# Performance work log

Hardware: AMD Instinct MI355X
Metric: run time of the kernel (lower is better)

## Reference

```python
import jax, jax.numpy as jnp
import numpy as np

N, E, B = 4096, 4096, 128  # nodes, edges, graphs


def _param(key, shape, scale):
    return jax.random.normal(key, shape, dtype=jnp.float32) * scale


def setup_inputs() -> dict:
    key = jax.random.key(0)
    ks = jax.random.split(key, 32)
    inp = {
        "x": jax.random.normal(ks[0], (N, 37), dtype=jnp.float32),
        "edge_index": jax.random.randint(ks[1], (2, E), 0, N),
        "edge_attr": jax.random.uniform(ks[2], (E, 5), dtype=jnp.float32),
        "batch": jnp.sort(jax.random.randint(ks[3], (N,), 0, B)),
        # NNConv 1: edge-MLP 5->512->37*128, root [37,128]
        "nn1_w1": _param(ks[4], (5, 512), 0.3),
        "nn1_b1": jnp.zeros((512,), jnp.float32),
        "nn1_w2": _param(ks[5], (512, 37 * 128), 0.01),
        "nn1_b2": jnp.zeros((37 * 128,), jnp.float32),
        "root1": _param(ks[6], (37, 128), 0.1),
        "bias1": jnp.zeros((128,), jnp.float32),
        # NNConv 2: edge-MLP 5->128->128*256, root [128,256]
        "nn2_w1": _param(ks[7], (5, 128), 0.3),
        "nn2_b1": jnp.zeros((128,), jnp.float32),
        "nn2_w2": _param(ks[8], (128, 128 * 256), 0.005),
        "nn2_b2": jnp.zeros((128 * 256,), jnp.float32),
        "root2": _param(ks[9], (128, 256), 0.05),
        "bias2": jnp.zeros((256,), jnp.float32),
        # NNConv 3: edge-MLP 5->128->256*256, root [256,256]
        "nn3_w1": _param(ks[10], (5, 128), 0.3),
        "nn3_b1": jnp.zeros((128,), jnp.float32),
        "nn3_w2": _param(ks[11], (128, 256 * 256), 0.005),
        "nn3_b2": jnp.zeros((256 * 256,), jnp.float32),
        "root3": _param(ks[12], (256, 256), 0.05),
        "bias3": jnp.zeros((256,), jnp.float32),
        # readout MLP
        "fc1_w": _param(ks[13], (256, 128), 0.06),
        "fc1_b": jnp.zeros((128,), jnp.float32),
        "fc2_w": _param(ks[14], (128, 64), 0.09),
        "fc2_b": jnp.zeros((64,), jnp.float32),
        "fc3_w": _param(ks[15], (64, 1), 0.12),
        "fc3_b": jnp.zeros((1,), jnp.float32),
    }
    return inp


def _nnconv(x, src, dst, edge_attr, w1, b1, w2, b2, root, bias, cin, cout):
    # edge MLP -> per-edge weight matrix [E, cin, cout]
    h = jax.nn.relu(edge_attr @ w1 + b1)
    W = (h @ w2 + b2).reshape(-1, cin, cout)
    # gather source features, per-edge matvec, scatter-add to targets
    msg = jnp.einsum('ei,eio->eo', x[src], W)          # [E, cout]
    agg = jax.ops.segment_sum(msg, dst, num_segments=x.shape[0])
    return agg + x @ root + bias


def _segment_mean(x, seg, num_segments):
    s = jax.ops.segment_sum(x, seg, num_segments=num_segments)
    cnt = jax.ops.segment_sum(jnp.ones((x.shape[0],), x.dtype), seg,
                              num_segments=num_segments)
    return s / jnp.maximum(cnt, 1.0)[:, None]


def reference(x, edge_index, edge_attr, batch,
              nn1_w1, nn1_b1, nn1_w2, nn1_b2, root1, bias1,
              nn2_w1, nn2_b1, nn2_w2, nn2_b2, root2, bias2,
              nn3_w1, nn3_b1, nn3_w2, nn3_b2, root3, bias3,
              fc1_w, fc1_b, fc2_w, fc2_b, fc3_w, fc3_b):
    src, dst = edge_index[0], edge_index[1]
    h = jax.nn.elu(_nnconv(x, src, dst, edge_attr, nn1_w1, nn1_b1, nn1_w2,
                           nn1_b2, root1, bias1, 37, 128))
    h = jax.nn.elu(_nnconv(h, src, dst, edge_attr, nn2_w1, nn2_b1, nn2_w2,
                           nn2_b2, root2, bias2, 128, 256))
    h = jax.nn.elu(_nnconv(h, src, dst, edge_attr, nn3_w1, nn3_b1, nn3_w2,
                           nn3_b2, root3, bias3, 256, 256))
    g = _segment_mean(h, batch, B)                     # [B, 256]
    g = jax.nn.elu(g @ fc1_w + fc1_b)
    g = jax.nn.elu(g @ fc2_w + fc2_b)
    g = g @ fc3_w + fc3_b
    return g.reshape(-1)
```

## Files before the change

### kernel.cpp

```cpp
#include <hip/hip_runtime.h>
#include <cstdint>
#include <cstddef>

typedef float f32x4 __attribute__((ext_vector_type(4)));
typedef _Float16 f16x8 __attribute__((ext_vector_type(8)));
typedef _Float16 f16x4 __attribute__((ext_vector_type(4)));
typedef _Float16 f16x2 __attribute__((ext_vector_type(2)));

__device__ __forceinline__ float elu_f(float x) { return x > 0.f ? x : expm1f(x); }

__device__ __forceinline__ void gload_lds16(const void* g, void* l)
{
    __builtin_amdgcn_global_load_lds(
        (const __attribute__((address_space(1))) void*)g,
        (__attribute__((address_space(3))) void*)l,
        16, 0, 0);
}

__global__ __launch_bounds__(256)
void edge_mlp_kernel(const float* __restrict__ ea,
                     const float* __restrict__ w1a, const float* __restrict__ b1a, float* __restrict__ h1T,
                     const float* __restrict__ w1b, const float* __restrict__ b1b, float* __restrict__ h2T,
                     const float* __restrict__ w1c, const float* __restrict__ b1c, float* __restrict__ h3T,
                     int E)
{
    const int e0  = blockIdx.x * 64;
    const int tid = threadIdx.x;
    const int el  = tid & 63;
    const int cg  = tid >> 6;
    __shared__ float a[64][5];
    for (int i = tid; i < 320; i += 256) a[i / 5][i % 5] = ea[e0 * 5 + i];
    __syncthreads();
    float av[5];
    #pragma unroll
    for (int j = 0; j < 5; ++j) av[j] = a[el][j];

    #pragma unroll 4
    for (int t = 0; t < 128; ++t) {
        const int ch = t * 4 + cg;
        float s = b1a[ch];
        #pragma unroll
        for (int j = 0; j < 5; ++j) s = fmaf(av[j], w1a[j * 512 + ch], s);
        h1T[(size_t)ch * E + e0 + el] = fmaxf(s, 0.f);
    }
    #pragma unroll 4
    for (int t = 0; t < 32; ++t) {
        const int ch = t * 4 + cg;
        float s = b1b[ch];
        float u = b1c[ch];
        #pragma unroll
        for (int j = 0; j < 5; ++j) {
            s = fmaf(av[j], w1b[j * 128 + ch], s);
            u = fmaf(av[j], w1c[j * 128 + ch], u);
        }
        h2T[(size_t)ch * E + e0 + el] = fmaxf(s, 0.f);
        h3T[(size_t)ch * E + e0 + el] = fmaxf(u, 0.f);
    }
}

template <int CIN, int COUT, int KFTOT>
__global__ __launch_bounds__(256)
void pack_w2_kernel(const float* __restrict__ w2, const float* __restrict__ b2,
                    _Float16* __restrict__ w2h, int KH)
{
    __shared__ float tile[32][COUT + 2];
    const int bid = blockIdx.x;
    const int kh  = bid / KFTOT;
    const int c   = bid - kh * KFTOT;
    const int tid = threadIdx.x;
    const int CP  = 32 * COUT;
    for (int i = tid; i < CP; i += 256) {
        int kk = i / COUT, n = i - kk * COUT;
        int kg = c * 32 + kk;
        float v = 0.f;
        if (kg < CIN) v = (kh < KH) ? w2[((size_t)kh * CIN + kg) * COUT + n]
                                    : b2[(size_t)kg * COUT + n];
        tile[kk][n] = v;
    }
    __syncthreads();
    _Float16* outp = w2h + (size_t)bid * CP;
    for (int i = tid; i < CP; i += 256) {
        int n = i >> 5, kk = i & 31;
        int blk = (kk >> 3) ^ ((n >> 1) & 3);
        outp[n * 32 + blk * 8 + (kk & 7)] = (_Float16)tile[kk][n];
    }
}

__global__ __launch_bounds__(256)
void csr_count_kernel(const int* __restrict__ dst, int* __restrict__ cnt, int E)
{
    int e = blockIdx.x * 256 + threadIdx.x;
    if (e < E) atomicAdd(&cnt[dst[e]], 1);
}

__global__ __launch_bounds__(256)
void csr_scan_kernel(const int* __restrict__ cnt, int* __restrict__ offs, int N)
{
    __shared__ int sums[256];
    __shared__ int pref[257];
    const int tid = threadIdx.x;
    const int per = N / 256;
    int loc = 0;
    for (int i = 0; i < per; ++i) loc += cnt[tid * per + i];
    sums[tid] = loc;
    __syncthreads();
    if (tid == 0) {
        int s = 0; pref[0] = 0;
        for (int i = 0; i < 256; ++i) { s += sums[i]; pref[i + 1] = s; }
    }
    __syncthreads();
    int run = pref[tid];
    for (int i = 0; i < per; ++i) { offs[tid * per + i] = run; run += cnt[tid * per + i]; }
    if (tid == 255) offs[N] = run;
}

__global__ __launch_bounds__(256)
void csr_fill_kernel(const int* __restrict__ dst, const int* __restrict__ offs,
                     int* __restrict__ cur, int* __restrict__ eid, int E)
{
    int e = blockIdx.x * 256 + threadIdx.x;
    if (e < E) {
        int d = dst[e];
        int p = offs[d] + atomicAdd(&cur[d], 1);
        eid[p] = e;
    }
}

__global__ __launch_bounds__(256)
void graph_offs_kernel(const int* __restrict__ batch, int* __restrict__ goffs, int N, int B)
{
    int g = blockIdx.x * 256 + threadIdx.x;
    if (g > B) return;
    int lo = 0, hi = N;
    while (lo < hi) { int mid = (lo + hi) >> 1; if (batch[mid] < g) lo = mid + 1; else hi = mid; }
    goffs[g] = lo;
}

template <int KH, int CIN, int COUT, int KFTOT, int CSPLIT, int NY>
__global__ __launch_bounds__(256, 2)
void msg_mfma_kernel(const float* __restrict__ xin,
                     const float* __restrict__ hT,
                     const _Float16* __restrict__ w2h,
                     const int* __restrict__ src,
                     _Float16* __restrict__ part,
                     int E, int khg_per)
{
    constexpr int BM = 256;
    constexpr int KF = KFTOT / CSPLIT;

    __shared__ __align__(16) _Float16 bsh[2][KF][64][32];
    __shared__ float s_h[2][BM];
    __shared__ int   s_src[BM];

    const int tid  = threadIdx.x;
    const int lane = tid & 63;
    const int w    = tid >> 6;
    const int l15  = lane & 15;
    const int lg   = lane >> 4;
    const int swb  = (l15 >> 1) & 3;

    const int nwg = gridDim.x;
    const int bid = blockIdx.x;
    const int swz = (bid & 7) * (nwg >> 3) + (bid >> 3);
    const int m    = swz & 15;
    const int rest = swz >> 4;
    const int y    = rest % NY;
    const int zz   = rest / NY;
    const int cinH = zz % CSPLIT;
    const int zkh  = zz / CSPLIT;

    const int e0  = m * BM;
    const int n0  = y * 64;
    const int k0  = cinH * KF * 32;
    const int kh0 = zkh * khg_per;
    const int kh1 = min(kh0 + khg_per, KH + 1);

    if (tid < BM) s_src[tid] = src[e0 + tid];
    __syncthreads();

    f16x8 a_[4][KF];
    #pragma unroll
    for (int mf = 0; mf < 4; ++mf) {
        const int eloc = w * 64 + mf * 16 + l15;
        const float* xrow = xin + (size_t)s_src[eloc] * CIN + k0;
        #pragma unroll
        for (int c = 0; c < KF; ++c) {
            if (CIN % 32 == 0) {
                float4 p0 = *(const float4*)(xrow + c * 32 + lg * 8);
                float4 p1 = *(const float4*)(xrow + c * 32 + lg * 8 + 4);
                a_[mf][c][0] = (_Float16)p0.x; a_[mf][c][1] = (_Float16)p0.y;
                a_[mf][c][2] = (_Float16)p0.z; a_[mf][c][3] = (_Float16)p0.w;
                a_[mf][c][4] = (_Float16)p1.x; a_[mf][c][5] = (_Float16)p1.y;
                a_[mf][c][6] = (_Float16)p1.z; a_[mf][c][7] = (_Float16)p1.w;
            } else {
                #pragma unroll
                for (int j = 0; j < 8; ++j) {
                    int kk = c * 32 + lg * 8 + j;
                    float v = (k0 + kk < CIN) ? xrow[kk] : 0.f;
                    a_[mf][c][j] = (_Float16)v;
                }
            }
        }
    }

    f32x4 msg[4][4];
    #pragma unroll
    for (int mf = 0; mf < 4; ++mf)
        #pragma unroll
        for (int nf = 0; nf < 4; ++nf) msg[mf][nf] = 0.f;

    auto stage = [&](int khg, int pp) {
        if (khg >= kh1) return;
        const size_t chunk0 = (size_t)khg * KFTOT + cinH * KF;
        const char* g = (const char*)(w2h + (chunk0 * COUT + n0) * 32) + (size_t)tid * 16;
        char* l = (char*)(&bsh[pp][0][0][0]) + (tid >> 6) * 1024;
        #pragma unroll
        for (int c = 0; c < KF; ++c)
            gload_lds16(g + (size_t)c * COUT * 64, l + c * 4096);
    };
    auto stage_h = [&](int khg) {
        if (khg < kh1 && khg < KH) s_h[khg & 1][tid] = hT[(size_t)khg * E + e0 + tid];
    };

    int p = 0;
    stage(kh0, 0);
    stage_h(kh0);

    for (int khg = kh0; khg < kh1; ++khg) {
        __syncthreads();

        stage(khg + 1, p ^ 1);
        stage_h(khg + 1);

        _Float16 hh[4];
        #pragma unroll
        for (int mf = 0; mf < 4; ++mf) {
            float hv = (khg < KH) ? s_h[khg & 1][w * 64 + mf * 16 + l15] : 1.f;
            hh[mf] = (_Float16)hv;
        }

        #pragma unroll
        for (int c = 0; c < KF; ++c) {
            f16x8 Bv[4];
            #pragma unroll
            for (int nf = 0; nf < 4; ++nf)
                Bv[nf] = *(const f16x8*)&bsh[p][c][nf * 16 + l15][(lg ^ swb) * 8];
            #pragma unroll
            for (int mf = 0; mf < 4; ++mf) {
                f16x8 ah = a_[mf][c] * hh[mf];
                #pragma unroll
                for (int nf = 0; nf < 4; ++nf)
                    msg[mf][nf] = __builtin_amdgcn_mfma_f32_16x16x32_f16(ah, Bv[nf], msg[mf][nf], 0, 0, 0);
            }
        }
        p ^= 1;
    }

    _Float16* pb = part + ((size_t)zz * E + e0) * COUT + n0;
    #pragma unroll
    for (int mf = 0; mf < 4; ++mf)
        #pragma unroll
        for (int r = 0; r < 4; ++r) {
            const int row = w * 64 + mf * 16 + lg * 4 + r;
            #pragma unroll
            for (int nf = 0; nf < 4; ++nf)
                pb[(size_t)row * COUT + nf * 16 + l15] = (_Float16)msg[mf][nf][r];
        }
}

template <int COUT, int Z>
__global__ __launch_bounds__(256)
void agg_gather_kernel(const _Float16* __restrict__ part, const int* __restrict__ offs,
                       const int* __restrict__ eid, float* __restrict__ agg, int E)
{
    constexpr int V = COUT / 64;
    const int n    = blockIdx.x * 4 + (threadIdx.x >> 6);
    const int lane = threadIdx.x & 63;
    float acc[V] = {};
    const int b = offs[n], t = offs[n + 1];
    for (int j = b; j < t; ++j) {
        const int e = eid[j];
        #pragma unroll
        for (int z = 0; z < Z; ++z) {
            const _Float16* row = part + ((size_t)z * E + e) * COUT + lane * V;
            if (V == 4) {
                f16x4 r4 = *(const f16x4*)row;
                acc[0] += (float)r4.x; acc[1] += (float)r4.y;
                acc[2] += (float)r4.z; acc[3] += (float)r4.w;
            } else {
                f16x2 r2 = *(const f16x2*)row;
                acc[0] += (float)r2.x; acc[1] += (float)r2.y;
            }
        }
    }
    float* o = agg + (size_t)n * COUT + lane * V;
    #pragma unroll
    for (int v = 0; v < V; ++v) o[v] = acc[v];
}

template <int CIN, int COUT>
__global__ __launch_bounds__(256)
void node_gemm_kernel(const float* __restrict__ xin,
                      const float* __restrict__ root,
                      const float* __restrict__ agg_in,
                      const float* __restrict__ bias,
                      float* __restrict__ out)
{
    constexpr int BM  = 64;
    constexpr int BN  = 64;
    constexpr int BKI = (CIN % 32 == 0) ? 32 : 16;
    constexpr int CIN_PAD = ((CIN + BKI - 1) / BKI) * BKI;
    constexpr int CPK = CIN_PAD / BKI;
    constexpr int NROWS = BKI / 16;

    __shared__ __align__(16) float xs_t[CIN_PAD][BM];
    __shared__ __align__(16) float btile[BKI][BN];

    const int tid = threadIdx.x;
    const int tx  = tid & 15;
    const int ty  = tid >> 4;
    const int ty4 = ty * 4;
    const int tx4 = tx * 4;
    const int e0  = blockIdx.x * BM;
    const int n0  = blockIdx.y * BN;

    for (int idx = tid; idx < BM * CIN_PAD; idx += 256) {
        int mm = idx / CIN_PAD;
        int i  = idx - mm * CIN_PAD;
        float v = 0.f;
        if (i < CIN) v = xin[(size_t)(e0 + mm) * CIN + i];
        xs_t[i][mm] = v;
    }

    const int rbase = tid >> 4;
    const int nn    = (tid & 15) * 4;
    float acc[4][4] = {};
    float4 pre[NROWS];

    {
        const float* brow = root + n0;
        #pragma unroll
        for (int rr = 0; rr < NROWS; ++rr) {
            int r = rbase + rr * 16;
            float4 v = {0.f, 0.f, 0.f, 0.f};
            if (r < CIN) v = *(const float4*)(brow + (size_t)r * COUT + nn);
            pre[rr] = v;
        }
    }

    for (int c = 0; c < CPK; ++c) {
        __syncthreads();
        #pragma unroll
        for (int rr = 0; rr < NROWS; ++rr)
            *(float4*)&btile[rbase + rr * 16][nn] = pre[rr];
        __syncthreads();

        if (c + 1 < CPK) {
            int i0n = (c + 1) * BKI;
            const float* brow = root + (size_t)i0n * COUT + n0;
            #pragma unroll
            for (int rr = 0; rr < NROWS; ++rr) {
                int r = rbase + rr * 16;
                float4 v = {0.f, 0.f, 0.f, 0.f};
                if (i0n + r < CIN) v = *(const float4*)(brow + (size_t)r * COUT + nn);
                pre[rr] = v;
            }
        }

        const int i0 = c * BKI;
        #pragma unroll
        for (int ii = 0; ii < BKI; ++ii) {
            float4 xv = *(const float4*)&xs_t[i0 + ii][ty4];
            float4 bv = *(const float4*)&btile[ii][tx4];
            float av[4] = {xv.x, xv.y, xv.z, xv.w};
            float bvv[4] = {bv.x, bv.y, bv.z, bv.w};
            #pragma unroll
            for (int mm = 0; mm < 4; ++mm)
                #pragma unroll
                for (int nq = 0; nq < 4; ++nq)
                    acc[mm][nq] = fmaf(av[mm], bvv[nq], acc[mm][nq]);
        }
    }

    float bs[4];
    #pragma unroll
    for (int nq = 0; nq < 4; ++nq) bs[nq] = bias[n0 + tx4 + nq];
    #pragma unroll
    for (int mm = 0; mm < 4; ++mm) {
        size_t base = (size_t)(e0 + ty4 + mm) * COUT + n0 + tx4;
        #pragma unroll
        for (int nq = 0; nq < 4; ++nq) {
            float v = acc[mm][nq] + agg_in[base + nq] + bs[nq];
            out[base + nq] = elu_f(v);
        }
    }
}

__global__ __launch_bounds__(256)
void pool_kernel(const float* __restrict__ hl3, const int* __restrict__ goffs,
                 float* __restrict__ gmean)
{
    const int g = blockIdx.x;
    const int c = threadIdx.x;
    const int b = goffs[g], t = goffs[g + 1];
    float s = 0.f;
    for (int n = b; n < t; ++n) s += hl3[(size_t)n * 256 + c];
    gmean[(size_t)g * 256 + c] = s / fmaxf((float)(t - b), 1.f);
}

__global__ __launch_bounds__(256)
void readout_kernel(const float* __restrict__ gmean,
                    const float* __restrict__ fc1w, const float* __restrict__ fc1b,
                    const float* __restrict__ fc2w, const float* __restrict__ fc2b,
                    const float* __restrict__ fc3w, const float* __restrict__ fc3b,
                    float* __restrict__ outp)
{
    const int g   = blockIdx.x;
    const int tid = threadIdx.x;
    __shared__ float gm[256];
    __shared__ float a1[128];
    __shared__ float a2[64];
    gm[tid] = gmean[(size_t)g * 256 + tid];
    __syncthreads();
    if (tid < 128) {
        float s = fc1b[tid];
        for (int j = 0; j < 256; ++j) s = fmaf(gm[j], fc1w[j * 128 + tid], s);
        a1[tid] = elu_f(s);
    }
    __syncthreads();
    if (tid < 64) {
        float s = fc2b[tid];
        for (int j = 0; j < 128; ++j) s = fmaf(a1[j], fc2w[j * 64 + tid], s);
        a2[tid] = elu_f(s);
    }
    __syncthreads();
    if (tid == 0) {
        float s = fc3b[0];
        for (int j = 0; j < 64; ++j) s = fmaf(a2[j], fc3w[j], s);
        outp[g] = s;
    }
}

extern "C" void kernel_launch(void* const* d_in, const int* in_sizes, int n_in,
                              void* d_out, int out_size, void* d_ws, size_t ws_size,
                              hipStream_t stream)
{
    const float* x      = (const float*)d_in[0];
    const int*   ei     = (const int*)  d_in[1];
    const float* ea     = (const float*)d_in[2];
    const int*   batch  = (const int*)  d_in[3];
    const float* nn1_w1 = (const float*)d_in[4];
    const float* nn1_b1 = (const float*)d_in[5];
    const float* nn1_w2 = (const float*)d_in[6];
    const float* nn1_b2 = (const float*)d_in[7];
    const float* root1  = (const float*)d_in[8];
    const float* bias1  = (const float*)d_in[9];
    const float* nn2_w1 = (const float*)d_in[10];
    const float* nn2_b1 = (const float*)d_in[11];
    const float* nn2_w2 = (const float*)d_in[12];
    const float* nn2_b2 = (const float*)d_in[13];
    const float* root2  = (const float*)d_in[14];
    const float* bias2  = (const float*)d_in[15];
    const float* nn3_w1 = (const float*)d_in[16];
    const float* nn3_b1 = (const float*)d_in[17];
    const float* nn3_w2 = (const float*)d_in[18];
    const float* nn3_b2 = (const float*)d_in[19];
    const float* root3  = (const float*)d_in[20];
    const float* bias3  = (const float*)d_in[21];
    const float* fc1_w  = (const float*)d_in[22];
    const float* fc1_b  = (const float*)d_in[23];
    const float* fc2_w  = (const float*)d_in[24];
    const float* fc2_b  = (const float*)d_in[25];
    const float* fc3_w  = (const float*)d_in[26];
    const float* fc3_b  = (const float*)d_in[27];

    const int E = in_sizes[2] / 5;
    const int N = in_sizes[0] / 37;
    const int B = out_size;
    const int* srcp = ei;
    const int* dstp = ei + E;

    const size_t W1H = (size_t)513 * 2 * 128 * 32;
    const size_t W2H = (size_t)129 * 4 * 256 * 32;
    const size_t W3H = (size_t)129 * 8 * 256 * 32;
    _Float16* w2h1 = (_Float16*)d_ws;
    _Float16* w2h2 = w2h1 + W1H;
    _Float16* w2h3 = w2h2 + W2H;
    float* fbase = (float*)(w2h3 + W3H);

    float* h1T   = fbase;
    float* h2T   = h1T + (size_t)512 * E;
    float* h3T   = h2T + (size_t)128 * E;
    float* hl1   = h3T + (size_t)128 * E;
    float* hl2   = hl1 + (size_t)N * 128;
    float* hl3   = hl2 + (size_t)N * 256;
    float* agg   = hl3 + (size_t)N * 256;
    float* gmean = agg + (size_t)N * 256;
    _Float16* part = (_Float16*)(gmean + (size_t)B * 256);
    int* ibase   = (int*)(part + (size_t)16 * E * 128);
    int* cnt   = ibase;
    int* cur   = cnt + N;
    int* offs  = cur + N;
    int* eid   = offs + N + 1;
    int* goffs = eid + E;

    hipMemsetAsync(cnt, 0, 2 * N * sizeof(int), stream);

    csr_count_kernel<<<(E + 255) / 256, 256, 0, stream>>>(dstp, cnt, E);
    csr_scan_kernel<<<1, 256, 0, stream>>>(cnt, offs, N);
    csr_fill_kernel<<<(E + 255) / 256, 256, 0, stream>>>(dstp, offs, cur, eid, E);
    graph_offs_kernel<<<1, 256, 0, stream>>>(batch, goffs, N, B);

    edge_mlp_kernel<<<E / 64, 256, 0, stream>>>(ea, nn1_w1, nn1_b1, h1T,
                                                nn2_w1, nn2_b1, h2T,
                                                nn3_w1, nn3_b1, h3T, E);

    pack_w2_kernel<37, 128, 2><<<513 * 2, 256, 0, stream>>>(nn1_w2, nn1_b2, w2h1, 512);
    pack_w2_kernel<128, 256, 4><<<129 * 4, 256, 0, stream>>>(nn2_w2, nn2_b2, w2h2, 128);
    pack_w2_kernel<256, 256, 8><<<129 * 8, 256, 0, stream>>>(nn3_w2, nn3_b2, w2h3, 128);

    msg_mfma_kernel<512, 37, 128, 2, 1, 2><<<512, 256, 0, stream>>>(
        x, h1T, w2h1, srcp, part, E, 33);
    agg_gather_kernel<128, 16><<<N / 4, 256, 0, stream>>>(part, offs, eid, agg, E);
    node_gemm_kernel<37, 128><<<dim3(N / 64, 2), 256, 0, stream>>>(
        x, root1, agg, bias1, hl1);

    msg_mfma_kernel<128, 128, 256, 4, 1, 4><<<512, 256, 0, stream>>>(
        hl1, h2T, w2h2, srcp, part, E, 17);
    agg_gather_kernel<256, 8><<<N / 4, 256, 0, stream>>>(part, offs, eid, agg, E);
    node_gemm_kernel<128, 256><<<dim3(N / 64, 4), 256, 0, stream>>>(
        hl1, root2, agg, bias2, hl2);

    msg_mfma_kernel<128, 256, 256, 8, 2, 4><<<512, 256, 0, stream>>>(
        hl2, h3T, w2h3, srcp, part, E, 33);
    agg_gather_kernel<256, 8><<<N / 4, 256, 0, stream>>>(part, offs, eid, agg, E);
    node_gemm_kernel<256, 256><<<dim3(N / 64, 4), 256, 0, stream>>>(
        hl2, root3, agg, bias3, hl3);

    pool_kernel<<<B, 256, 0, stream>>>(hl3, goffs, gmean);
    readout_kernel<<<B, 256, 0, stream>>>(gmean, fc1_w, fc1_b,
                                          fc2_w, fc2_b, fc3_w, fc3_b,
                                          (float*)d_out);
}
```

Measured before the change: 346.4 us.

## Fuse CSR build, aggregation and pooling kernels; halve msg tile rows; fp16 edge hidden

Folds the destination-count atomics into the edge-MLP kernel. Merges the CSR scan with the graph-offset search, and merges pooling with the readout MLP. The separate aggregation kernel is removed: the node GEMM epilogue now gathers and sums the fp16 partial messages per node directly. The edge hidden activations are stored in fp16, and the message MFMA kernel uses 128-edge tiles with a doubled grid and a higher occupancy target. Together these cut launch count, intermediate fp32 round trips and memory traffic, at the cost of a serial per-row gather inside the node GEMM epilogue and extra rounding of the hidden values.

```diff
diff --git a/kernel.cpp b/kernel.cpp
--- a/kernel.cpp
+++ b/kernel.cpp
@@ -5,7 +5,6 @@
 typedef float f32x4 __attribute__((ext_vector_type(4)));
 typedef _Float16 f16x8 __attribute__((ext_vector_type(8)));
 typedef _Float16 f16x4 __attribute__((ext_vector_type(4)));
-typedef _Float16 f16x2 __attribute__((ext_vector_type(2)));
 
 __device__ __forceinline__ float elu_f(float x) { return x > 0.f ? x : expm1f(x); }
 
@@ -19,15 +18,17 @@
 
 __global__ __launch_bounds__(256)
 void edge_mlp_kernel(const float* __restrict__ ea,
-                     const float* __restrict__ w1a, const float* __restrict__ b1a, float* __restrict__ h1T,
-                     const float* __restrict__ w1b, const float* __restrict__ b1b, float* __restrict__ h2T,
-                     const float* __restrict__ w1c, const float* __restrict__ b1c, float* __restrict__ h3T,
+                     const int* __restrict__ dst, int* __restrict__ cnt,
+                     const float* __restrict__ w1a, const float* __restrict__ b1a, _Float16* __restrict__ h1T,
+                     const float* __restrict__ w1b, const float* __restrict__ b1b, _Float16* __restrict__ h2T,
+                     const float* __restrict__ w1c, const float* __restrict__ b1c, _Float16* __restrict__ h3T,
                      int E)
 {
     const int e0  = blockIdx.x * 64;
     const int tid = threadIdx.x;
     const int el  = tid & 63;
     const int cg  = tid >> 6;
+    if (tid < 64) atomicAdd(&cnt[dst[e0 + tid]], 1);
     __shared__ float a[64][5];
     for (int i = tid; i < 320; i += 256) a[i / 5][i % 5] = ea[e0 * 5 + i];
     __syncthreads();
@@ -41,7 +42,7 @@
         float s = b1a[ch];
         #pragma unroll
         for (int j = 0; j < 5; ++j) s = fmaf(av[j], w1a[j * 512 + ch], s);
-        h1T[(size_t)ch * E + e0 + el] = fmaxf(s, 0.f);
+        h1T[(size_t)ch * E + e0 + el] = (_Float16)fmaxf(s, 0.f);
     }
     #pragma unroll 4
     for (int t = 0; t < 32; ++t) {
@@ -53,8 +54,8 @@
             s = fmaf(av[j], w1b[j * 128 + ch], s);
             u = fmaf(av[j], w1c[j * 128 + ch], u);
         }
-        h2T[(size_t)ch * E + e0 + el] = fmaxf(s, 0.f);
-        h3T[(size_t)ch * E + e0 + el] = fmaxf(u, 0.f);
+        h2T[(size_t)ch * E + e0 + el] = (_Float16)fmaxf(s, 0.f);
+        h3T[(size_t)ch * E + e0 + el] = (_Float16)fmaxf(u, 0.f);
     }
 }
 
@@ -87,14 +88,9 @@
 }
 
 __global__ __launch_bounds__(256)
-void csr_count_kernel(const int* __restrict__ dst, int* __restrict__ cnt, int E)
-{
-    int e = blockIdx.x * 256 + threadIdx.x;
-    if (e < E) atomicAdd(&cnt[dst[e]], 1);
-}
-
-__global__ __launch_bounds__(256)
-void csr_scan_kernel(const int* __restrict__ cnt, int* __restrict__ offs, int N)
+void csr_scan_graph_kernel(const int* __restrict__ cnt, int* __restrict__ offs, int N,
+                           const int* __restrict__ batch, int* __restrict__ goffs, int B,
+                           int NN)
 {
     __shared__ int sums[256];
     __shared__ int pref[257];
@@ -112,6 +108,11 @@
     int run = pref[tid];
     for (int i = 0; i < per; ++i) { offs[tid * per + i] = run; run += cnt[tid * per + i]; }
     if (tid == 255) offs[N] = run;
+    for (int g = tid; g <= B; g += 256) {
+        int lo = 0, hi = NN;
+        while (lo < hi) { int mid = (lo + hi) >> 1; if (batch[mid] < g) lo = mid + 1; else hi = mid; }
+        goffs[g] = lo;
+    }
 }
 
 __global__ __launch_bounds__(256)
@@ -126,31 +127,21 @@
     }
 }
 
-__global__ __launch_bounds__(256)
-void graph_offs_kernel(const int* __restrict__ batch, int* __restrict__ goffs, int N, int B)
-{
-    int g = blockIdx.x * 256 + threadIdx.x;
-    if (g > B) return;
-    int lo = 0, hi = N;
-    while (lo < hi) { int mid = (lo + hi) >> 1; if (batch[mid] < g) lo = mid + 1; else hi = mid; }
-    goffs[g] = lo;
-}
-
 template <int KH, int CIN, int COUT, int KFTOT, int CSPLIT, int NY>
-__global__ __launch_bounds__(256, 2)
+__global__ __launch_bounds__(256, 4)
 void msg_mfma_kernel(const float* __restrict__ xin,
-                     const float* __restrict__ hT,
+                     const _Float16* __restrict__ hT,
                      const _Float16* __restrict__ w2h,
                      const int* __restrict__ src,
                      _Float16* __restrict__ part,
                      int E, int khg_per)
 {
-    constexpr int BM = 256;
+    constexpr int BM = 128;
     constexpr int KF = KFTOT / CSPLIT;
 
     __shared__ __align__(16) _Float16 bsh[2][KF][64][32];
-    __shared__ float s_h[2][BM];
-    __shared__ int   s_src[BM];
+    __shared__ _Float16 s_h[2][BM];
+    __shared__ int s_src[BM];
 
     const int tid  = threadIdx.x;
     const int lane = tid & 63;
@@ -162,8 +153,8 @@
     const int nwg = gridDim.x;
     const int bid = blockIdx.x;
     const int swz = (bid & 7) * (nwg >> 3) + (bid >> 3);
-    const int m    = swz & 15;
-    const int rest = swz >> 4;
+    const int m    = swz & 31;
+    const int rest = swz >> 5;
     const int y    = rest % NY;
     const int zz   = rest / NY;
     const int cinH = zz % CSPLIT;
@@ -178,10 +169,10 @@
     if (tid < BM) s_src[tid] = src[e0 + tid];
     __syncthreads();
 
-    f16x8 a_[4][KF];
+    f16x8 a_[2][KF];
     #pragma unroll
-    for (int mf = 0; mf < 4; ++mf) {
-        const int eloc = w * 64 + mf * 16 + l15;
+    for (int mf = 0; mf < 2; ++mf) {
+        const int eloc = w * 32 + mf * 16 + l15;
         const float* xrow = xin + (size_t)s_src[eloc] * CIN + k0;
         #pragma unroll
         for (int c = 0; c < KF; ++c) {
@@ -203,9 +194,9 @@
         }
     }
 
-    f32x4 msg[4][4];
+    f32x4 msg[2][4];
     #pragma unroll
-    for (int mf = 0; mf < 4; ++mf)
+    for (int mf = 0; mf < 2; ++mf)
         #pragma unroll
         for (int nf = 0; nf < 4; ++nf) msg[mf][nf] = 0.f;
 
@@ -219,7 +210,8 @@
             gload_lds16(g + (size_t)c * COUT * 64, l + c * 4096);
     };
     auto stage_h = [&](int khg) {
-        if (khg < kh1 && khg < KH) s_h[khg & 1][tid] = hT[(size_t)khg * E + e0 + tid];
+        if (tid < BM && khg < kh1 && khg < KH)
+            s_h[khg & 1][tid] = hT[(size_t)khg * E + e0 + tid];
     };
 
     int p = 0;
@@ -232,12 +224,10 @@
         stage(khg + 1, p ^ 1);
         stage_h(khg + 1);
 
-        _Float16 hh[4];
-        #pragma unroll
-        for (int mf = 0; mf < 4; ++mf) {
-            float hv = (khg < KH) ? s_h[khg & 1][w * 64 + mf * 16 + l15] : 1.f;
-            hh[mf] = (_Float16)hv;
-        }
+        _Float16 hh[2];
+        #pragma unroll
+        for (int mf = 0; mf < 2; ++mf)
+            hh[mf] = (khg < KH) ? s_h[khg & 1][w * 32 + mf * 16 + l15] : (_Float16)1.0f;
 
         #pragma unroll
         for (int c = 0; c < KF; ++c) {
@@ -246,7 +236,7 @@
             for (int nf = 0; nf < 4; ++nf)
                 Bv[nf] = *(const f16x8*)&bsh[p][c][nf * 16 + l15][(lg ^ swb) * 8];
             #pragma unroll
-            for (int mf = 0; mf < 4; ++mf) {
+            for (int mf = 0; mf < 2; ++mf) {
                 f16x8 ah = a_[mf][c] * hh[mf];
                 #pragma unroll
                 for (int nf = 0; nf < 4; ++nf)
@@ -258,53 +248,25 @@
 
     _Float16* pb = part + ((size_t)zz * E + e0) * COUT + n0;
     #pragma unroll
-    for (int mf = 0; mf < 4; ++mf)
+    for (int mf = 0; mf < 2; ++mf)
         #pragma unroll
         for (int r = 0; r < 4; ++r) {
-            const int row = w * 64 + mf * 16 + lg * 4 + r;
+            const int row = w * 32 + mf * 16 + lg * 4 + r;
             #pragma unroll
             for (int nf = 0; nf < 4; ++nf)
                 pb[(size_t)row * COUT + nf * 16 + l15] = (_Float16)msg[mf][nf][r];
         }
 }
 
-template <int COUT, int Z>
-__global__ __launch_bounds__(256)
-void agg_gather_kernel(const _Float16* __restrict__ part, const int* __restrict__ offs,
-                       const int* __restrict__ eid, float* __restrict__ agg, int E)
-{
-    constexpr int V = COUT / 64;
-    const int n    = blockIdx.x * 4 + (threadIdx.x >> 6);
-    const int lane = threadIdx.x & 63;
-    float acc[V] = {};
-    const int b = offs[n], t = offs[n + 1];
-    for (int j = b; j < t; ++j) {
-        const int e = eid[j];
-        #pragma unroll
-        for (int z = 0; z < Z; ++z) {
-            const _Float16* row = part + ((size_t)z * E + e) * COUT + lane * V;
-            if (V == 4) {
-                f16x4 r4 = *(const f16x4*)row;
-                acc[0] += (float)r4.x; acc[1] += (float)r4.y;
-                acc[2] += (float)r4.z; acc[3] += (float)r4.w;
-            } else {
-                f16x2 r2 = *(const f16x2*)row;
-                acc[0] += (float)r2.x; acc[1] += (float)r2.y;
-            }
-        }
-    }
-    float* o = agg + (size_t)n * COUT + lane * V;
-    #pragma unroll
-    for (int v = 0; v < V; ++v) o[v] = acc[v];
-}
-
-template <int CIN, int COUT>
+template <int CIN, int COUT, int Z>
 __global__ __launch_bounds__(256)
 void node_gemm_kernel(const float* __restrict__ xin,
                       const float* __restrict__ root,
-                      const float* __restrict__ agg_in,
+                      const _Float16* __restrict__ part,
+                      const int* __restrict__ offs,
+                      const int* __restrict__ eid,
                       const float* __restrict__ bias,
-                      float* __restrict__ out)
+                      float* __restrict__ out, int E)
 {
     constexpr int BM  = 64;
     constexpr int BN  = 64;
@@ -385,59 +347,61 @@
     float bs[4];
     #pragma unroll
     for (int nq = 0; nq < 4; ++nq) bs[nq] = bias[n0 + tx4 + nq];
+
     #pragma unroll
     for (int mm = 0; mm < 4; ++mm) {
-        size_t base = (size_t)(e0 + ty4 + mm) * COUT + n0 + tx4;
-        #pragma unroll
-        for (int nq = 0; nq < 4; ++nq) {
-            float v = acc[mm][nq] + agg_in[base + nq] + bs[nq];
-            out[base + nq] = elu_f(v);
-        }
+        const int row = e0 + ty4 + mm;
+        float add[4] = {0.f, 0.f, 0.f, 0.f};
+        const int b = offs[row], t = offs[row + 1];
+        for (int j = b; j < t; ++j) {
+            const int e = eid[j];
+            #pragma unroll
+            for (int z = 0; z < Z; ++z) {
+                f16x4 r4 = *(const f16x4*)(part + ((size_t)z * E + e) * COUT + n0 + tx4);
+                add[0] += (float)r4.x; add[1] += (float)r4.y;
+                add[2] += (float)r4.z; add[3] += (float)r4.w;
+            }
+        }
+        size_t base = (size_t)row * COUT + n0 + tx4;
+        #pragma unroll
+        for (int nq = 0; nq < 4; ++nq)
+            out[base + nq] = elu_f(acc[mm][nq] + add[nq] + bs[nq]);
     }
 }
 
 __global__ __launch_bounds__(256)
-void pool_kernel(const float* __restrict__ hl3, const int* __restrict__ goffs,
-                 float* __restrict__ gmean)
-{
-    const int g = blockIdx.x;
-    const int c = threadIdx.x;
-    const int b = goffs[g], t = goffs[g + 1];
-    float s = 0.f;
-    for (int n = b; n < t; ++n) s += hl3[(size_t)n * 256 + c];
-    gmean[(size_t)g * 256 + c] = s / fmaxf((float)(t - b), 1.f);
-}
-
-__global__ __launch_bounds__(256)
-void readout_kernel(const float* __restrict__ gmean,
-                    const float* __restrict__ fc1w, const float* __restrict__ fc1b,
-                    const float* __restrict__ fc2w, const float* __restrict__ fc2b,
-                    const float* __restrict__ fc3w, const float* __restrict__ fc3b,
-                    float* __restrict__ outp)
+void pool_readout_kernel(const float* __restrict__ hl3, const int* __restrict__ goffs,
+                         const float* __restrict__ fc1w, const float* __restrict__ fc1b,
+                         const float* __restrict__ fc2w, const float* __restrict__ fc2b,
+                         const float* __restrict__ fc3w, const float* __restrict__ fc3b,
+                         float* __restrict__ outp)
 {
     const int g   = blockIdx.x;
     const int tid = threadIdx.x;
     __shared__ float gm[256];
     __shared__ float a1[128];
     __shared__ float a2[64];
-    gm[tid] = gmean[(size_t)g * 256 + tid];
+    const int b = goffs[g], t = goffs[g + 1];
+    float s = 0.f;
+    for (int n = b; n < t; ++n) s += hl3[(size_t)n * 256 + tid];
+    gm[tid] = s / fmaxf((float)(t - b), 1.f);
     __syncthreads();
     if (tid < 128) {
-        float s = fc1b[tid];
-        for (int j = 0; j < 256; ++j) s = fmaf(gm[j], fc1w[j * 128 + tid], s);
-        a1[tid] = elu_f(s);
+        float v = fc1b[tid];
+        for (int j = 0; j < 256; ++j) v = fmaf(gm[j], fc1w[j * 128 + tid], v);
+        a1[tid] = elu_f(v);
     }
     __syncthreads();
     if (tid < 64) {
-        float s = fc2b[tid];
-        for (int j = 0; j < 128; ++j) s = fmaf(a1[j], fc2w[j * 64 + tid], s);
-        a2[tid] = elu_f(s);
+        float v = fc2b[tid];
+        for (int j = 0; j < 128; ++j) v = fmaf(a1[j], fc2w[j * 64 + tid], v);
+        a2[tid] = elu_f(v);
     }
     __syncthreads();
     if (tid == 0) {
-        float s = fc3b[0];
-        for (int j = 0; j < 64; ++j) s = fmaf(a2[j], fc3w[j], s);
-        outp[g] = s;
+        float v = fc3b[0];
+        for (int j = 0; j < 64; ++j) v = fmaf(a2[j], fc3w[j], v);
+        outp[g] = v;
     }
 }
 
@@ -486,18 +450,15 @@
     _Float16* w2h1 = (_Float16*)d_ws;
     _Float16* w2h2 = w2h1 + W1H;
     _Float16* w2h3 = w2h2 + W2H;
-    float* fbase = (float*)(w2h3 + W3H);
-
-    float* h1T   = fbase;
-    float* h2T   = h1T + (size_t)512 * E;
-    float* h3T   = h2T + (size_t)128 * E;
-    float* hl1   = h3T + (size_t)128 * E;
+    _Float16* h1T  = w2h3 + W3H;
+    _Float16* h2T  = h1T + (size_t)512 * E;
+    _Float16* h3T  = h2T + (size_t)128 * E;
+    _Float16* part = h3T + (size_t)128 * E;
+    float* fbase = (float*)(part + (size_t)16 * E * 128);
+    float* hl1   = fbase;
     float* hl2   = hl1 + (size_t)N * 128;
     float* hl3   = hl2 + (size_t)N * 256;
-    float* agg   = hl3 + (size_t)N * 256;
-    float* gmean = agg + (size_t)N * 256;
-    _Float16* part = (_Float16*)(gmean + (size_t)B * 256);
-    int* ibase   = (int*)(part + (size_t)16 * E * 128);
+    int* ibase   = (int*)(hl3 + (size_t)N * 256);
     int* cnt   = ibase;
     int* cur   = cnt + N;
     int* offs  = cur + N;
@@ -506,12 +467,8 @@
 
     hipMemsetAsync(cnt, 0, 2 * N * sizeof(int), stream);
 
-    csr_count_kernel<<<(E + 255) / 256, 256, 0, stream>>>(dstp, cnt, E);
-    csr_scan_kernel<<<1, 256, 0, stream>>>(cnt, offs, N);
-    csr_fill_kernel<<<(E + 255) / 256, 256, 0, stream>>>(dstp, offs, cur, eid, E);
-    graph_offs_kernel<<<1, 256, 0, stream>>>(batch, goffs, N, B);
-
-    edge_mlp_kernel<<<E / 64, 256, 0, stream>>>(ea, nn1_w1, nn1_b1, h1T,
+    edge_mlp_kernel<<<E / 64, 256, 0, stream>>>(ea, dstp, cnt,
+                                                nn1_w1, nn1_b1, h1T,
                                                 nn2_w1, nn2_b1, h2T,
                                                 nn3_w1, nn3_b1, h3T, E);
 
@@ -519,26 +476,25 @@
     pack_w2_kernel<128, 256, 4><<<129 * 4, 256, 0, stream>>>(nn2_w2, nn2_b2, w2h2, 128);
     pack_w2_kernel<256, 256, 8><<<129 * 8, 256, 0, stream>>>(nn3_w2, nn3_b2, w2h3, 128);
 
-    msg_mfma_kernel<512, 37, 128, 2, 1, 2><<<512, 256, 0, stream>>>(
+    csr_scan_graph_kernel<<<1, 256, 0, stream>>>(cnt, offs, N, batch, goffs, B, N);
+    csr_fill_kernel<<<(E + 255) / 256, 256, 0, stream>>>(dstp, offs, cur, eid, E);
+
+    msg_mfma_kernel<512, 37, 128, 2, 1, 2><<<1024, 256, 0, stream>>>(
         x, h1T, w2h1, srcp, part, E, 33);
-    agg_gather_kernel<128, 16><<<N / 4, 256, 0, stream>>>(part, offs, eid, agg, E);
-    node_gemm_kernel<37, 128><<<dim3(N / 64, 2), 256, 0, stream>>>(
-        x, root1, agg, bias1, hl1);
-
-    msg_mfma_kernel<128, 128, 256, 4, 1, 4><<<512, 256, 0, stream>>>(
+    node_gemm_kernel<37, 128, 16><<<dim3(N / 64, 2), 256, 0, stream>>>(
+        x, root1, part, offs, eid, bias1, hl1, E);
+
+    msg_mfma_kernel<128, 128, 256, 4, 1, 4><<<1024, 256, 0, stream>>>(
         hl1, h2T, w2h2, srcp, part, E, 17);
-    agg_gather_kernel<256, 8><<<N / 4, 256, 0, stream>>>(part, offs, eid, agg, E);
-    node_gemm_kernel<128, 256><<<dim3(N / 64, 4), 256, 0, stream>>>(
-        hl1, root2, agg, bias2, hl2);
-
-    msg_mfma_kernel<128, 256, 256, 8, 2, 4><<<512, 256, 0, stream>>>(
+    node_gemm_kernel<128, 256, 8><<<dim3(N / 64, 4), 256, 0, stream>>>(
+        hl1, root2, part, offs, eid, bias2, hl2, E);
+
+    msg_mfma_kernel<128, 256, 256, 8, 2, 4><<<1024, 256, 0, stream>>>(
         hl2, h3T, w2h3, srcp, part, E, 33);
-    agg_gather_kernel<256, 8><<<N / 4, 256, 0, stream>>>(part, offs, eid, agg, E);
-    node_gemm_kernel<256, 256><<<dim3(N / 64, 4), 256, 0, stream>>>(
-        hl2, root3, agg, bias3, hl3);
-
-    pool_kernel<<<B, 256, 0, stream>>>(hl3, goffs, gmean);
-    readout_kernel<<<B, 256, 0, stream>>>(gmean, fc1_w, fc1_b,
-                                          fc2_w, fc2_b, fc3_w, fc3_b,
-                                          (float*)d_out);
-}
+    node_gemm_kernel<256, 256, 8><<<dim3(N / 64, 4), 256, 0, stream>>>(
+        hl2, root3, part, offs, eid, bias3, hl3, E);
+
+    pool_readout_kernel<<<B, 256, 0, stream>>>(hl3, goffs, fc1_w, fc1_b,
+                                               fc2_w, fc2_b, fc3_w, fc3_b,
+                                               (float*)d_out);
+}
```

Measured after the change: 312.4 us. 1.11x faster.
